# Kernel tuning notes

Hardware: AMD Instinct MI355X
Metric: run time of the kernel (lower is better)

Reference implementation:

```python
import jax, jax.numpy as jnp
import numpy as np

L = 4            # num_layers (experts)
D_IN = 2048
D_OUT = 2048
B = 16384        # tokens


def setup_inputs() -> dict:
    key = jax.random.key(0)
    k_x, k_idx, k_w, k_b = jax.random.split(key, 4)
    x = jax.random.normal(k_x, (B, D_IN), dtype=jnp.float32)
    layer_idx = jax.random.randint(k_idx, (B,), 0, L, dtype=jnp.int64)
    # Per-expert linear params. Torch Linear stores W as [out,in] and computes
    # x @ W.T + b; we store the equivalent [L, in, out] layout directly.
    bound = 1.0 / np.sqrt(D_IN)
    W = jax.random.uniform(k_w, (L, D_IN, D_OUT), jnp.float32, -bound, bound)
    b = jax.random.uniform(k_b, (L, D_OUT), jnp.float32, -bound, bound)
    return {"x": x, "layer_idx": layer_idx, "W": W, "b": b}


def reference(x, layer_idx, W, b):
    # Faithful to ParallelLinear.forward with layer_idx given: the
    # split -> per-group linear -> concat -> argsort-unpermute pipeline is
    # mathematically out[j] = x[j] @ W[layer_idx[j]] + b[layer_idx[j]].
    # Dense jit-friendly form: run every expert on all tokens, then select.
    all_out = jnp.einsum('bi,lio->lbo', x, W) + b[:, None, :]   # [L, B, out]
    tok = jnp.arange(x.shape[0])
    return all_out[layer_idx, tok]                              # [B, out]
```

## Files before the change

kernel.cpp:

```cpp
#include <hip/hip_runtime.h>
#include <stdint.h>

#define L_EXPERTS 4
#define D_IN  2048
#define D_OUT 2048
#define B_TOK 16384

using f32x4  = __attribute__((ext_vector_type(4))) float;
using bf16x8 = __attribute__((ext_vector_type(8))) short;

__device__ __forceinline__ uint32_t f2bf(float f) {
    union { float f; uint32_t u; } v; v.f = f;
    uint32_t u = v.u;
    return (u + 0x7fffu + ((u >> 16) & 1u)) >> 16;
}

__device__ __forceinline__ void gl_lds16(const void* g, void* l) {
    __builtin_amdgcn_global_load_lds(
        (const __attribute__((address_space(1))) void*)g,
        (__attribute__((address_space(3))) void*)l, 16, 0, 0);
}

__global__ void hist_kernel(const int* __restrict__ idx, int* __restrict__ hist) {
    __shared__ int h[L_EXPERTS];
    if (threadIdx.x < L_EXPERTS) h[threadIdx.x] = 0;
    __syncthreads();
    const int e = idx[blockIdx.x * 256 + threadIdx.x];
    atomicAdd(&h[e], 1);
    __syncthreads();
    if (threadIdx.x < L_EXPERTS)
        hist[blockIdx.x * L_EXPERTS + threadIdx.x] = h[threadIdx.x];
}

__global__ void prefix_kernel(const int* __restrict__ hist,
                              int* __restrict__ meta, int* __restrict__ cursor) {
    __shared__ int tot[L_EXPERTS];
    if (threadIdx.x < L_EXPERTS) {
        int s = 0;
        for (int b = 0; b < 64; ++b) s += hist[b * L_EXPERTS + threadIdx.x];
        tot[threadIdx.x] = s;
    }
    __syncthreads();
    if (threadIdx.x == 0) {
        int o = 0;
        for (int e = 0; e < L_EXPERTS; ++e) {
            meta[e] = o; cursor[e] = o; o += tot[e];
        }
        meta[L_EXPERTS] = o;
    }
}

__global__ void scatter_kernel(const int* __restrict__ idx,
                               int* __restrict__ cursor, int* __restrict__ perm) {
    const int i = blockIdx.x * 256 + threadIdx.x;
    const int e = idx[i];
    const int lane = threadIdx.x & 63;
    const unsigned long long lt_mask = (1ull << lane) - 1ull;
    int pos = 0;
    #pragma unroll
    for (int ee = 0; ee < L_EXPERTS; ++ee) {
        unsigned long long m = __ballot(e == ee);
        if (m) {
            int leader = __ffsll(m) - 1;
            int base = 0;
            if (lane == leader) base = atomicAdd(&cursor[ee], __popcll(m));
            base = __shfl(base, leader);
            if (e == ee) pos = base + __popcll(m & lt_mask);
        }
    }
    perm[pos] = i;
}

__global__ void gather_convert(const float* __restrict__ x,
                               const int* __restrict__ perm,
                               uint32_t* __restrict__ Ag) {
    const int p = blockIdx.x;
    const int t = perm[p];
    const float4* src = (const float4*)(x + (size_t)t * D_IN);
    uint4* dst = (uint4*)(Ag + (size_t)p * (D_IN / 2));
    const int j = threadIdx.x;
    float4 v0 = src[2 * j], v1 = src[2 * j + 1];
    uint4 o;
    o.x = f2bf(v0.x) | (f2bf(v0.y) << 16);
    o.y = f2bf(v0.z) | (f2bf(v0.w) << 16);
    o.z = f2bf(v1.x) | (f2bf(v1.y) << 16);
    o.w = f2bf(v1.z) | (f2bf(v1.w) << 16);
    dst[j] = o;
}

__global__ void wtrans(const float* __restrict__ W, ushort* __restrict__ Wt) {
    __shared__ float tile[64][65];
    const int l  = blockIdx.z;
    const int k0 = blockIdx.x * 64, n0 = blockIdx.y * 64;
    const float* Wl = W + (size_t)l * D_IN * D_OUT;
    ushort* Wtl = Wt + (size_t)l * D_IN * D_OUT;
    const int t = threadIdx.x;
    const int kr = t >> 4, nc = (t & 15) * 4;
    #pragma unroll
    for (int i = 0; i < 64; i += 16) {
        float4 v = *(const float4*)&Wl[(size_t)(k0 + kr + i) * D_OUT + n0 + nc];
        tile[kr + i][nc]     = v.x; tile[kr + i][nc + 1] = v.y;
        tile[kr + i][nc + 2] = v.z; tile[kr + i][nc + 3] = v.w;
    }
    __syncthreads();
    const int nr = t >> 3, kc = (t & 7) * 8;
    #pragma unroll
    for (int i = 0; i < 64; i += 32) {
        uint4 o;
        o.x = f2bf(tile[kc + 0][nr + i]) | (f2bf(tile[kc + 1][nr + i]) << 16);
        o.y = f2bf(tile[kc + 2][nr + i]) | (f2bf(tile[kc + 3][nr + i]) << 16);
        o.z = f2bf(tile[kc + 4][nr + i]) | (f2bf(tile[kc + 5][nr + i]) << 16);
        o.w = f2bf(tile[kc + 6][nr + i]) | (f2bf(tile[kc + 7][nr + i]) << 16);
        *(uint4*)&Wtl[(size_t)(n0 + nr + i) * D_IN + k0 + kc] = o;
    }
}

__global__ __launch_bounds__(256, 3)
void gemm_grouped(const ushort* __restrict__ Ag, const ushort* __restrict__ Wt,
                  const float* __restrict__ bias, const int* __restrict__ meta,
                  const int* __restrict__ perm, float* __restrict__ out) {
    __shared__ __align__(16) ushort smem[2 * 16 * 512];

    int off[L_EXPERTS + 1];
    #pragma unroll
    for (int i = 0; i <= L_EXPERTS; ++i) off[i] = meta[i];

    const int gid = blockIdx.x;
    const int mt = (gid >> 7) * 8 + (gid & 7);
    const int nt = (gid & 127) >> 3;

    int e = -1, lt = 0, t0 = 0;
    #pragma unroll
    for (int i = 0; i < L_EXPERTS; ++i) {
        int cnt = off[i + 1] - off[i];
        int tiles = (cnt + 127) >> 7;
        if (e < 0 && mt < t0 + tiles) { e = i; lt = mt - t0; }
        t0 += tiles;
    }
    if (e < 0) return;
    const int rowbase = off[e] + lt * 128;
    const int cnt_e   = off[e + 1] - off[e];
    const int n0      = nt * 128;

    const int tid  = threadIdx.x;
    const int lane = tid & 63;
    const int w    = tid >> 6;
    const int wm   = w & 1, wn = w >> 1;
    const int l15  = lane & 15, lq = lane >> 4;

    const ushort* gp[4];
    #pragma unroll
    for (int q = 0; q < 4; ++q) {
        const int cidx = w * 4 + q;
        if (cidx < 8) {
            int row = rowbase + cidx * 16 + l15;
            gp[q] = Ag + (size_t)row * D_IN + lq * 8;
        } else {
            int col = n0 + (cidx - 8) * 16 + l15;
            gp[q] = Wt + ((size_t)e * D_OUT + col) * D_IN + lq * 8;
        }
    }

    f32x4 acc[4][4] = {};
    const int NK = D_IN / 32;

    #pragma unroll
    for (int q = 0; q < 4; ++q)
        gl_lds16(gp[q], &smem[(w * 4 + q) * 512]);
    __syncthreads();

    for (int k = 0; k < NK; ++k) {
        if (k + 1 < NK) {
            const int nb = (k + 1) & 1;
            #pragma unroll
            for (int q = 0; q < 4; ++q)
                gl_lds16(gp[q] + (k + 1) * 32,
                         &smem[(nb * 16 + w * 4 + q) * 512]);
        }
        const ushort* base = &smem[(k & 1) * 16 * 512];
        bf16x8 af[4], bg[4];
        #pragma unroll
        for (int i = 0; i < 4; ++i)
            af[i] = *(const bf16x8*)&base[(wm * 4 + i) * 512 + lane * 8];
        #pragma unroll
        for (int j = 0; j < 4; ++j)
            bg[j] = *(const bf16x8*)&base[(8 + wn * 4 + j) * 512 + lane * 8];
        #pragma unroll
        for (int i = 0; i < 4; ++i)
            #pragma unroll
            for (int j = 0; j < 4; ++j)
                acc[i][j] = __builtin_amdgcn_mfma_f32_16x16x32_bf16(
                    af[i], bg[j], acc[i][j], 0, 0, 0);
        __syncthreads();
    }

    float bv[4];
    #pragma unroll
    for (int j = 0; j < 4; ++j)
        bv[j] = bias[(size_t)e * D_OUT + n0 + wn * 64 + j * 16 + l15];
    #pragma unroll
    for (int i = 0; i < 4; ++i) {
        #pragma unroll
        for (int r = 0; r < 4; ++r) {
            int lr = lt * 128 + wm * 64 + i * 16 + lq * 4 + r;
            if (lr < cnt_e) {
                int tok = perm[off[e] + lr];
                float* orow = out + (size_t)tok * D_OUT + n0 + wn * 64 + l15;
                #pragma unroll
                for (int j = 0; j < 4; ++j)
                    orow[j * 16] = acc[i][j][r] + bv[j];
            }
        }
    }
}

__global__ void fallback_kernel(const float* __restrict__ x, const int* __restrict__ idx,
                                const float* __restrict__ W, const float* __restrict__ bias,
                                float* __restrict__ out) {
    __shared__ float xs[D_IN];
    const int t = blockIdx.x;
    const int e = idx[t];
    const float* xr = x + (size_t)t * D_IN;
    for (int k = threadIdx.x; k < D_IN; k += 256) xs[k] = xr[k];
    __syncthreads();
    const float* We = W + (size_t)e * D_IN * D_OUT;
    #pragma unroll 2
    for (int j = 0; j < D_OUT / 256; ++j) {
        int col = threadIdx.x + j * 256;
        float a = bias[(size_t)e * D_OUT + col];
        for (int k = 0; k < D_IN; ++k) a += xs[k] * We[(size_t)k * D_OUT + col];
        out[(size_t)t * D_OUT + col] = a;
    }
}

extern "C" void kernel_launch(void* const* d_in, const int* in_sizes, int n_in,
                              void* d_out, int out_size, void* d_ws, size_t ws_size,
                              hipStream_t stream) {
    const float* x   = (const float*)d_in[0];
    const int*   idx = (const int*)d_in[1];
    const float* W   = (const float*)d_in[2];
    const float* b   = (const float*)d_in[3];
    float* out = (float*)d_out;

    const size_t META_OFF = 0;
    const size_t PERM_OFF = 256;
    const size_t AG_OFF   = PERM_OFF + (size_t)B_TOK * 4;
    const size_t AG_BYTES = (size_t)(B_TOK + 128) * D_IN * 2;
    const size_t WT_OFF   = AG_OFF + AG_BYTES;
    const size_t WT_BYTES = (size_t)L_EXPERTS * D_IN * D_OUT * 2;
    const size_t NEED     = WT_OFF + WT_BYTES;

    if (ws_size < NEED) {
        fallback_kernel<<<B_TOK, 256, 0, stream>>>(x, idx, W, b, out);
        return;
    }

    int*      meta   = (int*)((char*)d_ws + META_OFF);
    int*      perm   = (int*)((char*)d_ws + PERM_OFF);
    int*      cursor = (int*)((char*)d_ws + AG_OFF);
    int*      hist   = (int*)((char*)d_ws + AG_OFF + 256);
    uint32_t* Ag     = (uint32_t*)((char*)d_ws + AG_OFF);
    ushort*   Wt     = (ushort*)((char*)d_ws + WT_OFF);

    hist_kernel   <<<64, 256, 0, stream>>>(idx, hist);
    prefix_kernel <<<1, 64, 0, stream>>>(hist, meta, cursor);
    scatter_kernel<<<64, 256, 0, stream>>>(idx, cursor, perm);
    gather_convert<<<B_TOK, 256, 0, stream>>>(x, perm, Ag);
    wtrans        <<<dim3(32, 32, L_EXPERTS), 256, 0, stream>>>(W, Wt);
    gemm_grouped  <<<17 * 128, 256, 0, stream>>>(
        (const ushort*)Ag, Wt, b, meta, perm, out);
}
```

Measured before the change: 570.1 us.

## Enlarge grouped GEMM tile to 256x256 and make token scatter atomic-free

The grouped GEMM moves from 128x128 tiles with 256 threads to 256x256 tiles with 512 threads. Each of the 8 waves now computes a 128x64 sub-tile, which doubles LDS and accumulator usage but raises operand reuse per load. Routing now uses per-block prefix bases computed in prefix_kernel instead of atomics, so the token permutation becomes deterministic. The gather/convert kernel switches to a grid-stride loop over 4096 blocks. The bigger tiles cut the GEMM grid to 544 blocks, which risks a worse tail and lower occupancy from register pressure.

```diff
diff --git a/kernel.cpp b/kernel.cpp
--- a/kernel.cpp
+++ b/kernel.cpp
@@ -33,59 +33,79 @@
 }
 
 __global__ void prefix_kernel(const int* __restrict__ hist,
-                              int* __restrict__ meta, int* __restrict__ cursor) {
+                              int* __restrict__ meta, int* __restrict__ bbase) {
+    __shared__ int h[64][L_EXPERTS];
     __shared__ int tot[L_EXPERTS];
+    const int b = threadIdx.x >> 2, e = threadIdx.x & 3;
+    h[b][e] = hist[b * L_EXPERTS + e];
+    __syncthreads();
     if (threadIdx.x < L_EXPERTS) {
         int s = 0;
-        for (int b = 0; b < 64; ++b) s += hist[b * L_EXPERTS + threadIdx.x];
+        for (int bb = 0; bb < 64; ++bb) s += h[bb][threadIdx.x];
         tot[threadIdx.x] = s;
     }
     __syncthreads();
     if (threadIdx.x == 0) {
         int o = 0;
-        for (int e = 0; e < L_EXPERTS; ++e) {
-            meta[e] = o; cursor[e] = o; o += tot[e];
-        }
+        for (int ee = 0; ee < L_EXPERTS; ++ee) { meta[ee] = o; o += tot[ee]; }
         meta[L_EXPERTS] = o;
     }
+    if (threadIdx.x < L_EXPERTS) {
+        const int ee = threadIdx.x;
+        int base = 0;
+        for (int e3 = 0; e3 < ee; ++e3) base += tot[e3];
+        int run = base;
+        for (int bb = 0; bb < 64; ++bb) {
+            bbase[bb * L_EXPERTS + ee] = run;
+            run += h[bb][ee];
+        }
+    }
 }
 
 __global__ void scatter_kernel(const int* __restrict__ idx,
-                               int* __restrict__ cursor, int* __restrict__ perm) {
+                               const int* __restrict__ bbase,
+                               int* __restrict__ perm) {
+    __shared__ int wcnt[4][L_EXPERTS];
+    __shared__ int wbase[4][L_EXPERTS];
     const int i = blockIdx.x * 256 + threadIdx.x;
     const int e = idx[i];
+    const int w = threadIdx.x >> 6;
     const int lane = threadIdx.x & 63;
     const unsigned long long lt_mask = (1ull << lane) - 1ull;
-    int pos = 0;
+    int my_off = 0;
     #pragma unroll
     for (int ee = 0; ee < L_EXPERTS; ++ee) {
         unsigned long long m = __ballot(e == ee);
-        if (m) {
-            int leader = __ffsll(m) - 1;
-            int base = 0;
-            if (lane == leader) base = atomicAdd(&cursor[ee], __popcll(m));
-            base = __shfl(base, leader);
-            if (e == ee) pos = base + __popcll(m & lt_mask);
-        }
-    }
-    perm[pos] = i;
+        if (lane == 0) wcnt[w][ee] = __popcll(m);
+        if (e == ee) my_off = __popcll(m & lt_mask);
+    }
+    __syncthreads();
+    if (threadIdx.x < L_EXPERTS) {
+        const int ee = threadIdx.x;
+        int run = bbase[blockIdx.x * L_EXPERTS + ee];
+        #pragma unroll
+        for (int ww = 0; ww < 4; ++ww) { wbase[ww][ee] = run; run += wcnt[ww][ee]; }
+    }
+    __syncthreads();
+    perm[wbase[w][e] + my_off] = i;
 }
 
 __global__ void gather_convert(const float* __restrict__ x,
                                const int* __restrict__ perm,
                                uint32_t* __restrict__ Ag) {
-    const int p = blockIdx.x;
-    const int t = perm[p];
-    const float4* src = (const float4*)(x + (size_t)t * D_IN);
-    uint4* dst = (uint4*)(Ag + (size_t)p * (D_IN / 2));
     const int j = threadIdx.x;
-    float4 v0 = src[2 * j], v1 = src[2 * j + 1];
-    uint4 o;
-    o.x = f2bf(v0.x) | (f2bf(v0.y) << 16);
-    o.y = f2bf(v0.z) | (f2bf(v0.w) << 16);
-    o.z = f2bf(v1.x) | (f2bf(v1.y) << 16);
-    o.w = f2bf(v1.z) | (f2bf(v1.w) << 16);
-    dst[j] = o;
+    for (int p = blockIdx.x; p < B_TOK; p += gridDim.x) {
+        const int t = perm[p];
+        const float4* src = (const float4*)(x + (size_t)t * D_IN);
+        uint4* dst = (uint4*)(Ag + (size_t)p * (D_IN / 2));
+        float4 v0 = src[2 * j], v1 = src[2 * j + 1];
+        uint4 o;
+        o.x = f2bf(v0.x) | (f2bf(v0.y) << 16);
+        o.y = f2bf(v0.z) | (f2bf(v0.w) << 16);
+        o.z = f2bf(v1.x) | (f2bf(v1.y) << 16);
+        o.w = f2bf(v1.z) | (f2bf(v1.w) << 16);
+        dst[j] = o;
+    }
 }
 
 __global__ void wtrans(const float* __restrict__ W, ushort* __restrict__ Wt) {
@@ -115,32 +135,32 @@
     }
 }
 
-__global__ __launch_bounds__(256, 3)
+__global__ __launch_bounds__(512, 2)
 void gemm_grouped(const ushort* __restrict__ Ag, const ushort* __restrict__ Wt,
                   const float* __restrict__ bias, const int* __restrict__ meta,
                   const int* __restrict__ perm, float* __restrict__ out) {
-    __shared__ __align__(16) ushort smem[2 * 16 * 512];
+    __shared__ __align__(16) ushort smem[2 * 32 * 512];
 
     int off[L_EXPERTS + 1];
     #pragma unroll
     for (int i = 0; i <= L_EXPERTS; ++i) off[i] = meta[i];
 
     const int gid = blockIdx.x;
-    const int mt = (gid >> 7) * 8 + (gid & 7);
-    const int nt = (gid & 127) >> 3;
+    const int nt = gid & 7;
+    const int mt = gid >> 3;
 
     int e = -1, lt = 0, t0 = 0;
     #pragma unroll
     for (int i = 0; i < L_EXPERTS; ++i) {
         int cnt = off[i + 1] - off[i];
-        int tiles = (cnt + 127) >> 7;
+        int tiles = (cnt + 255) >> 8;
         if (e < 0 && mt < t0 + tiles) { e = i; lt = mt - t0; }
         t0 += tiles;
     }
     if (e < 0) return;
-    const int rowbase = off[e] + lt * 128;
+    const int rowbase = off[e] + lt * 256;
     const int cnt_e   = off[e + 1] - off[e];
-    const int n0      = nt * 128;
+    const int n0      = nt * 256;
 
     const int tid  = threadIdx.x;
     const int lane = tid & 63;
@@ -152,16 +172,17 @@
     #pragma unroll
     for (int q = 0; q < 4; ++q) {
         const int cidx = w * 4 + q;
-        if (cidx < 8) {
+        if (cidx < 16) {
             int row = rowbase + cidx * 16 + l15;
+            if (row > B_TOK + 127) row = B_TOK + 127;
             gp[q] = Ag + (size_t)row * D_IN + lq * 8;
         } else {
-            int col = n0 + (cidx - 8) * 16 + l15;
+            int col = n0 + (cidx - 16) * 16 + l15;
             gp[q] = Wt + ((size_t)e * D_OUT + col) * D_IN + lq * 8;
         }
     }
 
-    f32x4 acc[4][4] = {};
+    f32x4 acc[8][4] = {};
     const int NK = D_IN / 32;
 
     #pragma unroll
@@ -175,18 +196,18 @@
             #pragma unroll
             for (int q = 0; q < 4; ++q)
                 gl_lds16(gp[q] + (k + 1) * 32,
-                         &smem[(nb * 16 + w * 4 + q) * 512]);
-        }
-        const ushort* base = &smem[(k & 1) * 16 * 512];
-        bf16x8 af[4], bg[4];
-        #pragma unroll
-        for (int i = 0; i < 4; ++i)
-            af[i] = *(const bf16x8*)&base[(wm * 4 + i) * 512 + lane * 8];
+                         &smem[(nb * 32 + w * 4 + q) * 512]);
+        }
+        const ushort* base = &smem[(k & 1) * 32 * 512];
+        bf16x8 af[8], bg[4];
+        #pragma unroll
+        for (int i = 0; i < 8; ++i)
+            af[i] = *(const bf16x8*)&base[(wm * 8 + i) * 512 + lane * 8];
         #pragma unroll
         for (int j = 0; j < 4; ++j)
-            bg[j] = *(const bf16x8*)&base[(8 + wn * 4 + j) * 512 + lane * 8];
-        #pragma unroll
-        for (int i = 0; i < 4; ++i)
+            bg[j] = *(const bf16x8*)&base[(16 + wn * 4 + j) * 512 + lane * 8];
+        #pragma unroll
+        for (int i = 0; i < 8; ++i)
             #pragma unroll
             for (int j = 0; j < 4; ++j)
                 acc[i][j] = __builtin_amdgcn_mfma_f32_16x16x32_bf16(
@@ -199,10 +220,10 @@
     for (int j = 0; j < 4; ++j)
         bv[j] = bias[(size_t)e * D_OUT + n0 + wn * 64 + j * 16 + l15];
     #pragma unroll
-    for (int i = 0; i < 4; ++i) {
+    for (int i = 0; i < 8; ++i) {
         #pragma unroll
         for (int r = 0; r < 4; ++r) {
-            int lr = lt * 128 + wm * 64 + i * 16 + lq * 4 + r;
+            int lr = lt * 256 + wm * 128 + i * 16 + lq * 4 + r;
             if (lr < cnt_e) {
                 int tok = perm[off[e] + lr];
                 float* orow = out + (size_t)tok * D_OUT + n0 + wn * 64 + l15;
@@ -257,16 +278,16 @@
 
     int*      meta   = (int*)((char*)d_ws + META_OFF);
     int*      perm   = (int*)((char*)d_ws + PERM_OFF);
-    int*      cursor = (int*)((char*)d_ws + AG_OFF);
-    int*      hist   = (int*)((char*)d_ws + AG_OFF + 256);
+    int*      hist   = (int*)((char*)d_ws + AG_OFF);
+    int*      bbase  = (int*)((char*)d_ws + AG_OFF + 1024);
     uint32_t* Ag     = (uint32_t*)((char*)d_ws + AG_OFF);
     ushort*   Wt     = (ushort*)((char*)d_ws + WT_OFF);
 
     hist_kernel   <<<64, 256, 0, stream>>>(idx, hist);
-    prefix_kernel <<<1, 64, 0, stream>>>(hist, meta, cursor);
-    scatter_kernel<<<64, 256, 0, stream>>>(idx, cursor, perm);
-    gather_convert<<<B_TOK, 256, 0, stream>>>(x, perm, Ag);
+    prefix_kernel <<<1, 256, 0, stream>>>(hist, meta, bbase);
+    scatter_kernel<<<64, 256, 0, stream>>>(idx, bbase, perm);
+    gather_convert<<<4096, 256, 0, stream>>>(x, perm, Ag);
     wtrans        <<<dim3(32, 32, L_EXPERTS), 256, 0, stream>>>(W, Wt);
-    gemm_grouped  <<<17 * 128, 256, 0, stream>>>(
+    gemm_grouped  <<<68 * 8, 512, 0, stream>>>(
         (const ushort*)Ag, Wt, b, meta, perm, out);
 }
```

Result: faster. 544.5 us (-4.5%).
